# Optimization experiments

Measured on AMD Instinct MI355X. Metric: run time of the kernel, lower is better.

The kernel has to match this reference:

```python
import jax, jax.numpy as jnp
import numpy as np

MUL0, MUL1, SCALARS_OUT = 16, 16, 128
L0, L1 = MUL0, MUL1 * 3            # 16, 48
PATH_NUMEL = MUL0 * MUL1 * SCALARS_OUT  # 32768 per path, two paths
EPS = 1e-5
# e3nn normalization: irrep_normalization='component' -> alpha = dim(ir_out) = 1;
# path_normalization='element' -> divide by sum over paths to same output of mul1*mul2 = 256+256 = 512.
PATH_COEFF = 1.0 / np.sqrt(512.0)
CG_110 = 1.0 / np.sqrt(3.0)  # wigner_3j(1,1,0)[i,j] = delta_ij/sqrt(3) (unit Frobenius norm)


def layer_norm(x, g, b):
    mu = jnp.mean(x, axis=-1, keepdims=True)
    var = jnp.mean(jnp.square(x - mu), axis=-1, keepdims=True)
    return (x - mu) * jax.lax.rsqrt(var + EPS) * g + b


def ff_block(x, g, b, w1, w2, b2):
    # LayerNorm -> Linear(no bias) -> SiLU -> Linear(bias); residual=False in both uses
    h = jax.nn.silu(layer_norm(x, g, b) @ w1)
    return h @ w2 + b2


def setup_inputs() -> dict:
    key = jax.random.key(0)
    ks = jax.random.split(key, 8)
    N = 2048
    return {
        "x": jax.random.normal(ks[0], (N, L0 + L1), dtype=jnp.float32),
        "we_ln_g": jnp.ones((L0,), jnp.float32),
        "we_ln_b": jnp.zeros((L0,), jnp.float32),
        "we_w1": jax.random.normal(ks[1], (L0, 4 * L0), jnp.float32) / np.sqrt(L0),
        "we_w2": jax.random.normal(ks[2], (4 * L0, 2 * PATH_NUMEL), jnp.float32) / np.sqrt(4 * L0),
        "we_b2": jnp.zeros((2 * PATH_NUMEL,), jnp.float32),
        "om_ln_g": jnp.ones((SCALARS_OUT,), jnp.float32),
        "om_ln_b": jnp.zeros((SCALARS_OUT,), jnp.float32),
        "om_w1": jax.random.normal(ks[3], (SCALARS_OUT, 4 * SCALARS_OUT), jnp.float32) / np.sqrt(SCALARS_OUT),
        "om_w2": jax.random.normal(ks[4], (4 * SCALARS_OUT, 1), jnp.float32) / np.sqrt(4 * SCALARS_OUT),
        "om_b2": jnp.zeros((1,), jnp.float32),
    }


def reference(x, we_ln_g, we_ln_b, we_w1, we_w2, we_b2,
              om_ln_g, om_ln_b, om_w1, om_w2, om_b2):
    N = x.shape[0]
    feats = x[:, :L0]                       # [N, 16] scalars (0e)
    x1 = x[:, L0:].reshape(N, MUL1, 3)      # [N, 16, 3] vectors (1o)

    # per-sample tensor-product weights (shared_weights=False)
    w = ff_block(feats, we_ln_g, we_ln_b, we_w1, we_w2, we_b2)  # [N, 65536]
    w0 = w[:, :PATH_NUMEL].reshape(N, MUL0, MUL0, SCALARS_OUT)
    w1 = w[:, PATH_NUMEL:].reshape(N, MUL1, MUL1, SCALARS_OUT)

    # path 0: 0e x 0e -> 0e  (uvw)
    o0 = jnp.einsum('nu,nv,nuvw->nw', feats, feats, w0)
    # path 1: 1o x 1o -> 0e  (uvw, CG = delta_ij/sqrt(3))
    o1 = jnp.einsum('nui,nvi,nuvw->nw', x1, x1, w1) * CG_110
    tp_out = PATH_COEFF * (o0 + o1)          # [N, 128]

    return ff_block(tp_out, om_ln_g, om_ln_b, om_w1, om_w2, om_b2)  # [N, 1]
```

## Files before the change

kernel.cpp:

```cpp
#include <hip/hip_runtime.h>
#include <hip/hip_bf16.h>
#include <cstdint>

#define EPS 1e-5f
#define PATH_COEFF 0.04419417382415922f
#define CG110     0.5773502691896258f

typedef __bf16 v8bf __attribute__((ext_vector_type(8)));
typedef float  v4f  __attribute__((ext_vector_type(4)));
typedef _Float16 v4h __attribute__((ext_vector_type(4)));

static __device__ __forceinline__ unsigned short f2bf(float x){
    unsigned int u = __builtin_bit_cast(unsigned int, x);
    u += 0x7fffu + ((u >> 16) & 1u);
    return (unsigned short)(u >> 16);
}
static __device__ __forceinline__ unsigned short f2h(float x){
    return __builtin_bit_cast(unsigned short, (_Float16)x);
}

__global__ __launch_bounds__(256)
void k_pre(const float* __restrict__ w2, const float* __restrict__ b2,
           unsigned short* __restrict__ Vt2,
           const float* __restrict__ om_w1, unsigned short* __restrict__ w1t,
           const float* __restrict__ x, const float* __restrict__ lng,
           const float* __restrict__ lnb, const float* __restrict__ we_w1,
           unsigned short* __restrict__ Q2, float* __restrict__ Ht, int N)
{
    __shared__ __align__(16) unsigned short tile[32][128];
    int b = blockIdx.x;
    int t = threadIdx.x;

    if (b < 260){
        int k    = b >> 2;
        int slab = b & 3;
        const float* srcbase = (k < 64) ? (w2 + (size_t)k * 65536) : b2;
        for (int chunk = 0; chunk < 4; ++chunk){
            int pbase = slab*128 + chunk*32;
            #pragma unroll
            for (int i = 0; i < 4; ++i){
                int g = t + 256*i;
                int ploc = g >> 5, c4 = g & 31;
                const float4 v = *(const float4*)(srcbase + (size_t)(pbase + ploc)*128 + c4*4);
                unsigned int w0 = (unsigned)f2bf(v.x) | ((unsigned)f2bf(v.y) << 16);
                unsigned int w1 = (unsigned)f2bf(v.z) | ((unsigned)f2bf(v.w) << 16);
                *(uint2*)&tile[ploc][c4*4] = make_uint2(w0, w1);
            }
            __syncthreads();
            int w = t & 127, h = t >> 7;
            int ps = slab*4 + chunk;
            unsigned int words[8];
            #pragma unroll
            for (int g2 = 0; g2 < 8; ++g2)
                words[g2] = (unsigned)tile[h*16 + g2*2][w] | ((unsigned)tile[h*16 + g2*2 + 1][w] << 16);
            unsigned short* dq0 = Vt2 + (((size_t)(k*16 + ps)*4 + 2*h    )*128 + w)*8;
            unsigned short* dq1 = Vt2 + (((size_t)(k*16 + ps)*4 + 2*h + 1)*128 + w)*8;
            *(uint4*)dq0 = make_uint4(words[0], words[1], words[2], words[3]);
            *(uint4*)dq1 = make_uint4(words[4], words[5], words[6], words[7]);
            __syncthreads();
        }
    } else if (b < 264){
        int j0 = (b - 260) * 128;
        for (int chunk = 0; chunk < 4; ++chunk){
            #pragma unroll
            for (int i = 0; i < 4; ++i){
                int g = t + 256*i;
                int wloc = g >> 5, c4 = g & 31;
                int w = chunk*32 + wloc;
                const float4 v = *(const float4*)(om_w1 + (size_t)w*512 + j0 + c4*4);
                unsigned int a = (unsigned)f2bf(v.x) | ((unsigned)f2bf(v.y) << 16);
                unsigned int bb = (unsigned)f2bf(v.z) | ((unsigned)f2bf(v.w) << 16);
                *(uint2*)&tile[wloc][c4*4] = make_uint2(a, bb);
            }
            __syncthreads();
            int jl = t & 127, h = t >> 7;
            unsigned int words[8];
            #pragma unroll
            for (int g2 = 0; g2 < 8; ++g2)
                words[g2] = (unsigned)tile[h*16 + g2*2][jl] | ((unsigned)tile[h*16 + g2*2 + 1][jl] << 16);
            unsigned short* dst = w1t + (size_t)(j0 + jl)*128 + chunk*32 + h*16;
            *(uint4*)dst       = make_uint4(words[0], words[1], words[2], words[3]);
            *(uint4*)(dst + 8) = make_uint4(words[4], words[5], words[6], words[7]);
            __syncthreads();
        }
    } else {
        int wv = t >> 6, lane = t & 63;
        int row = (b - 264)*4 + wv;
        const float* xr = x + (size_t)row * 64;
        float f[16]; float mu = 0.f;
        #pragma unroll
        for (int u = 0; u < 16; ++u){ f[u] = xr[u]; mu += f[u]; }
        mu *= (1.f/16.f);
        float var = 0.f;
        #pragma unroll
        for (int u = 0; u < 16; ++u){ float d = f[u] - mu; var += d*d; }
        var *= (1.f/16.f);
        float inv = rsqrtf(var + EPS);
        float lnf[16];
        #pragma unroll
        for (int u = 0; u < 16; ++u) lnf[u] = (f[u]-mu)*inv*lng[u] + lnb[u];
        float h1 = 0.f;
        #pragma unroll
        for (int u = 0; u < 16; ++u) h1 += lnf[u] * we_w1[u*64 + lane];
        float h = h1 / (1.f + expf(-h1));
        Ht[(size_t)lane * N + row] = h;
        if (lane == 0) Ht[(size_t)64 * N + row] = 1.f;

        union { unsigned short qs[8]; uint4 v; } qu;
        #pragma unroll
        for (int j = 0; j < 8; ++j){
            int p = lane*8 + j;
            float q;
            if (p < 256){
                int u = p >> 4, v = p & 15;
                q = PATH_COEFF * f[u] * f[v];
            } else {
                int pp = p - 256;
                int u = pp >> 4, v = pp & 15;
                const float* ya = xr + 16 + u*3;
                const float* yb = xr + 16 + v*3;
                q = (PATH_COEFF * CG110) * (ya[0]*yb[0] + ya[1]*yb[1] + ya[2]*yb[2]);
            }
            qu.qs[j] = f2bf(q);
        }
        int rb = row >> 6, r64 = row & 63;
        int ps = lane >> 2, quad4 = lane & 3;
        *(uint4*)(Q2 + (((size_t)(rb*16 + ps)*4 + quad4)*64 + r64)*8) = qu.v;
    }
}

__global__ __launch_bounds__(256, 4)
void k_main(const unsigned short* __restrict__ Q2, const unsigned short* __restrict__ Vt2,
            const float* __restrict__ Ht, unsigned short* __restrict__ partial, int N)
{
    __shared__ __align__(16) unsigned short stile[4][64*72];
    int g = blockIdx.x & 7;
    int j = blockIdx.x >> 3;
    int kb, mb;
    if (j < 128){ mb = j >> 3; kb = g*8 + (j & 7); }
    else { if (g != 0) return; mb = j - 128; kb = 64; }

    int tid  = threadIdx.x;
    int lane = tid & 63, wv = tid >> 6;
    int r2 = wv >> 1, c2 = wv & 1;
    int quad = lane >> 4, l16 = lane & 15;
    int rowbase = mb*128 + r2*64;
    int rb = rowbase >> 6;
    int wbase = c2*64;

    const unsigned short* aroot = Q2  + (size_t)rb*32768 + quad*512  + l16*8;
    const unsigned short* broot = Vt2 + (size_t)kb*65536 + quad*1024 + (wbase + l16)*8;

    v4f acc[4][4];
    #pragma unroll
    for (int m=0;m<4;++m)
      #pragma unroll
      for (int n=0;n<4;++n)
        #pragma unroll
        for (int r=0;r<4;++r) acc[m][n][r] = 0.f;

    #pragma unroll 4
    for (int ps = 0; ps < 16; ++ps){
        const unsigned short* ap = aroot + ps*2048;
        const unsigned short* bp = broot + ps*4096;
        v8bf a[4], bb[4];
        #pragma unroll
        for (int m=0;m<4;++m) a[m]  = *(const v8bf*)(ap + m*128);
        #pragma unroll
        for (int n=0;n<4;++n) bb[n] = *(const v8bf*)(bp + n*128);
        #pragma unroll
        for (int m=0;m<4;++m)
          #pragma unroll
          for (int n=0;n<4;++n)
            acc[m][n] = __builtin_amdgcn_mfma_f32_16x16x32_bf16(a[m], bb[n], acc[m][n], 0, 0, 0);
    }

    const float* hp = Ht + (size_t)kb*N + rowbase + quad*4;
    unsigned short* my = stile[wv];
    #pragma unroll
    for (int m=0;m<4;++m){
        v4f hv = *(const v4f*)(hp + m*16);
        #pragma unroll
        for (int n=0;n<4;++n)
          #pragma unroll
          for (int r=0;r<4;++r)
            my[(m*16 + quad*4 + r)*72 + n*16 + l16] = f2h(hv[r]*acc[m][n][r]);
    }
    unsigned short* gp = partial + (size_t)kb*N*128 + (size_t)rowbase*128 + wbase;
    #pragma unroll
    for (int i = 0; i < 8; ++i){
        int row = i*8 + (lane >> 3);
        int c16 = (lane & 7)*8;
        uint4 v = *(const uint4*)&my[row*72 + c16];
        *(uint4*)(gp + (size_t)row*128 + c16) = v;
    }
}

__global__ __launch_bounds__(128)
void k_red(const unsigned short* __restrict__ partial, const float* __restrict__ g,
           const float* __restrict__ b, unsigned short* __restrict__ lnf, int N)
{
    int t = threadIdx.x;
    int row0 = blockIdx.x * 4;
    int rl = t >> 5, w = (t & 31)*4;
    int row = row0 + rl;

    const unsigned short* p0 = partial + (size_t)row*128 + w;
    float s0=0.f, s1=0.f, s2=0.f, s3=0.f;
    #pragma unroll
    for (int sl = 0; sl < 65; ++sl){
        v4h v = *(const v4h*)(p0 + (size_t)sl*N*128);
        s0 += (float)v[0]; s1 += (float)v[1]; s2 += (float)v[2]; s3 += (float)v[3];
    }
    float sum = s0+s1+s2+s3;
    float sq  = s0*s0+s1*s1+s2*s2+s3*s3;
    #pragma unroll
    for (int off=16; off>0; off>>=1){
        sum += __shfl_xor(sum, off, 32);
        sq  += __shfl_xor(sq,  off, 32);
    }
    float mu  = sum * (1.f/128.f);
    float var = sq * (1.f/128.f) - mu*mu;
    float inv = rsqrtf(var + EPS);
    unsigned short o[4];
    o[0] = f2bf((s0-mu)*inv*g[w+0] + b[w+0]);
    o[1] = f2bf((s1-mu)*inv*g[w+1] + b[w+1]);
    o[2] = f2bf((s2-mu)*inv*g[w+2] + b[w+2]);
    o[3] = f2bf((s3-mu)*inv*g[w+3] + b[w+3]);
    *(uint2*)(lnf + (size_t)row*128 + w) = *(uint2*)o;
}

__global__ __launch_bounds__(256)
void k_mlp2(const unsigned short* __restrict__ lnf, const unsigned short* __restrict__ w1t,
            const float* __restrict__ w2, const float* __restrict__ b2,
            float* __restrict__ out, int N)
{
    __shared__ float red2[4][64];
    int tid = threadIdx.x, lane = tid & 63, wv = tid >> 6;
    int quad = lane >> 4, l16 = lane & 15;
    int rowbase = blockIdx.x * 64;
    int jbase = wv * 128;

    v4f acc[4][8];
    #pragma unroll
    for (int m=0;m<4;++m)
      #pragma unroll
      for (int n=0;n<8;++n)
        #pragma unroll
        for (int r=0;r<4;++r) acc[m][n][r] = 0.f;

    #pragma unroll
    for (int ps = 0; ps < 4; ++ps){
        v8bf a[4], bb[8];
        #pragma unroll
        for (int m=0;m<4;++m)
            a[m]  = *(const v8bf*)(lnf + (size_t)(rowbase + m*16 + l16)*128 + ps*32 + quad*8);
        #pragma unroll
        for (int n=0;n<8;++n)
            bb[n] = *(const v8bf*)(w1t + (size_t)(jbase + n*16 + l16)*128 + ps*32 + quad*8);
        #pragma unroll
        for (int m=0;m<4;++m)
          #pragma unroll
          for (int n=0;n<8;++n)
            acc[m][n] = __builtin_amdgcn_mfma_f32_16x16x32_bf16(a[m], bb[n], acc[m][n], 0, 0, 0);
    }

    float w2v[8];
    #pragma unroll
    for (int n=0;n<8;++n) w2v[n] = w2[jbase + n*16 + l16];

    #pragma unroll
    for (int m=0;m<4;++m){
        #pragma unroll
        for (int r=0;r<4;++r){
            float s = 0.f;
            #pragma unroll
            for (int n=0;n<8;++n){
                float v = acc[m][n][r];
                s += (v / (1.f + expf(-v))) * w2v[n];
            }
            #pragma unroll
            for (int off=8; off>0; off>>=1) s += __shfl_xor(s, off, 16);
            if (l16 == 0) red2[wv][m*16 + quad*4 + r] = s;
        }
    }
    __syncthreads();
    if (tid < 64)
        out[rowbase + tid] = red2[0][tid] + red2[1][tid] + red2[2][tid] + red2[3][tid] + b2[0];
}

extern "C" void kernel_launch(void* const* d_in, const int* in_sizes, int n_in,
                              void* d_out, int out_size, void* d_ws, size_t ws_size,
                              hipStream_t stream)
{
    const float* x     = (const float*)d_in[0];
    const float* we_g  = (const float*)d_in[1];
    const float* we_b  = (const float*)d_in[2];
    const float* we_w1 = (const float*)d_in[3];
    const float* we_w2 = (const float*)d_in[4];
    const float* we_b2 = (const float*)d_in[5];
    const float* om_g  = (const float*)d_in[6];
    const float* om_b  = (const float*)d_in[7];
    const float* om_w1 = (const float*)d_in[8];
    const float* om_w2 = (const float*)d_in[9];
    const float* om_b2 = (const float*)d_in[10];

    int N  = in_sizes[0] / 64;

    char* ws = (char*)d_ws;
    size_t offV = 0;
    size_t szV  = (size_t)65*16*4*128*8*2;
    size_t offQ = offV + szV;
    size_t szQ  = (size_t)N*512*2;
    size_t offH = offQ + szQ;
    size_t szH  = (size_t)65*N*4;
    size_t offP = offH + szH;
    size_t szP  = (size_t)65*N*128*2;
    size_t offL = offP + szP;
    size_t szL  = (size_t)N*128*2;
    size_t offW = offL + szL;

    unsigned short* Vt2 = (unsigned short*)(ws + offV);
    unsigned short* Q2  = (unsigned short*)(ws + offQ);
    float* Ht           = (float*)(ws + offH);
    unsigned short* Par = (unsigned short*)(ws + offP);
    unsigned short* Lnf = (unsigned short*)(ws + offL);
    unsigned short* W1t = (unsigned short*)(ws + offW);
    float* out = (float*)d_out;

    hipLaunchKernelGGL(k_pre,  dim3(264 + N/4), dim3(256), 0, stream,
                       we_w2, we_b2, Vt2, om_w1, W1t, x, we_g, we_b, we_w1, Q2, Ht, N);
    hipLaunchKernelGGL(k_main, dim3(144*8),     dim3(256), 0, stream, Q2, Vt2, Ht, Par, N);
    hipLaunchKernelGGL(k_red,  dim3(N/4),       dim3(128), 0, stream, Par, om_g, om_b, Lnf, N);
    hipLaunchKernelGGL(k_mlp2, dim3(N/64),      dim3(256), 0, stream, Lnf, W1t, om_w2, om_b2, out, N);
}
```

Baseline: 145.8 us.

## Stage per-slice weight tile in LDS and process two row tiles per block

k_main now copies the kb weight slice from Vt2 into 64 KB of shared memory in two halves. Each block computes two 128-row tiles against it, so the B operand is reused from LDS instead of being re-read from global/L2 by every row tile. The grid shrinks to 65*8 blocks with launch bounds lowered to 2 per SM. The epilogue stages results through a smaller per-wave LDS buffer with a stride of 66, which can leave 16-byte LDS reads unaligned. Lower occupancy and fewer blocks may reduce latency hiding.

```diff
diff --git a/kernel.cpp b/kernel.cpp
--- a/kernel.cpp
+++ b/kernel.cpp
@@ -129,70 +129,93 @@
     }
 }
 
-__global__ __launch_bounds__(256, 4)
+__global__ __launch_bounds__(256, 2)
 void k_main(const unsigned short* __restrict__ Q2, const unsigned short* __restrict__ Vt2,
             const float* __restrict__ Ht, unsigned short* __restrict__ partial, int N)
 {
-    __shared__ __align__(16) unsigned short stile[4][64*72];
-    int g = blockIdx.x & 7;
-    int j = blockIdx.x >> 3;
-    int kb, mb;
-    if (j < 128){ mb = j >> 3; kb = g*8 + (j & 7); }
-    else { if (g != 0) return; mb = j - 128; kb = 64; }
+    __shared__ __align__(16) unsigned short Bs[32768];
+    int kb = blockIdx.x % 65;
+    int g  = blockIdx.x / 65;
 
     int tid  = threadIdx.x;
     int lane = tid & 63, wv = tid >> 6;
     int r2 = wv >> 1, c2 = wv & 1;
     int quad = lane >> 4, l16 = lane & 15;
-    int rowbase = mb*128 + r2*64;
-    int rb = rowbase >> 6;
     int wbase = c2*64;
 
-    const unsigned short* aroot = Q2  + (size_t)rb*32768 + quad*512  + l16*8;
-    const unsigned short* broot = Vt2 + (size_t)kb*65536 + quad*1024 + (wbase + l16)*8;
-
-    v4f acc[4][4];
-    #pragma unroll
-    for (int m=0;m<4;++m)
+    v4f acc[2][4][4];
+    #pragma unroll
+    for (int mi=0;mi<2;++mi)
       #pragma unroll
-      for (int n=0;n<4;++n)
-        #pragma unroll
-        for (int r=0;r<4;++r) acc[m][n][r] = 0.f;
-
-    #pragma unroll 4
-    for (int ps = 0; ps < 16; ++ps){
-        const unsigned short* ap = aroot + ps*2048;
-        const unsigned short* bp = broot + ps*4096;
-        v8bf a[4], bb[4];
-        #pragma unroll
-        for (int m=0;m<4;++m) a[m]  = *(const v8bf*)(ap + m*128);
-        #pragma unroll
-        for (int n=0;n<4;++n) bb[n] = *(const v8bf*)(bp + n*128);
-        #pragma unroll
-        for (int m=0;m<4;++m)
-          #pragma unroll
-          for (int n=0;n<4;++n)
-            acc[m][n] = __builtin_amdgcn_mfma_f32_16x16x32_bf16(a[m], bb[n], acc[m][n], 0, 0, 0);
-    }
-
-    const float* hp = Ht + (size_t)kb*N + rowbase + quad*4;
-    unsigned short* my = stile[wv];
-    #pragma unroll
-    for (int m=0;m<4;++m){
-        v4f hv = *(const v4f*)(hp + m*16);
+      for (int m=0;m<4;++m)
         #pragma unroll
         for (int n=0;n<4;++n)
           #pragma unroll
-          for (int r=0;r<4;++r)
-            my[(m*16 + quad*4 + r)*72 + n*16 + l16] = f2h(hv[r]*acc[m][n][r]);
-    }
-    unsigned short* gp = partial + (size_t)kb*N*128 + (size_t)rowbase*128 + wbase;
-    #pragma unroll
-    for (int i = 0; i < 8; ++i){
-        int row = i*8 + (lane >> 3);
-        int c16 = (lane & 7)*8;
-        uint4 v = *(const uint4*)&my[row*72 + c16];
-        *(uint4*)(gp + (size_t)row*128 + c16) = v;
+          for (int r=0;r<4;++r) acc[mi][m][n][r] = 0.f;
+
+    const unsigned short* bsrc = Vt2 + (size_t)kb*65536;
+
+    for (int half = 0; half < 2; ++half){
+        __syncthreads();
+        const uint4* s4 = (const uint4*)(bsrc + half*32768);
+        uint4* d4 = (uint4*)Bs;
+        #pragma unroll
+        for (int i = 0; i < 16; ++i)
+            d4[tid + i*256] = s4[tid + i*256];
+        __syncthreads();
+
+        #pragma unroll
+        for (int mi = 0; mi < 2; ++mi){
+            int rowbase = (g*2 + mi)*128 + r2*64;
+            int rb = rowbase >> 6;
+            const unsigned short* aroot = Q2 + (size_t)rb*32768 + half*16384 + quad*512 + l16*8;
+            #pragma unroll
+            for (int pc = 0; pc < 2; ++pc){
+                v8bf a[4][4];
+                #pragma unroll
+                for (int ps = 0; ps < 4; ++ps)
+                    #pragma unroll
+                    for (int m = 0; m < 4; ++m)
+                        a[ps][m] = *(const v8bf*)(aroot + (pc*4 + ps)*2048 + m*128);
+                #pragma unroll
+                for (int ps = 0; ps < 4; ++ps){
+                    int ps8 = pc*4 + ps;
+                    const unsigned short* bp = Bs + ((ps8*4 + quad)*128 + wbase + l16)*8;
+                    v8bf bb[4];
+                    #pragma unroll
+                    for (int n = 0; n < 4; ++n) bb[n] = *(const v8bf*)(bp + n*128);
+                    #pragma unroll
+                    for (int m = 0; m < 4; ++m)
+                      #pragma unroll
+                      for (int n = 0; n < 4; ++n)
+                        acc[mi][m][n] = __builtin_amdgcn_mfma_f32_16x16x32_bf16(a[ps][m], bb[n], acc[mi][m][n], 0, 0, 0);
+                }
+            }
+        }
+    }
+
+    __syncthreads();
+    unsigned short* Es = Bs + wv*1056;
+    #pragma unroll
+    for (int mi = 0; mi < 2; ++mi){
+        int rowbase = (g*2 + mi)*128 + r2*64;
+        const float* hp = Ht + (size_t)kb*N + rowbase + quad*4;
+        #pragma unroll
+        for (int m = 0; m < 4; ++m){
+            v4f hv = *(const v4f*)(hp + m*16);
+            #pragma unroll
+            for (int n = 0; n < 4; ++n)
+              #pragma unroll
+              for (int r = 0; r < 4; ++r)
+                Es[(quad*4 + r)*66 + n*16 + l16] = f2h(hv[r]*acc[mi][m][n][r]);
+            unsigned short* gp = partial + (size_t)kb*N*128 + (size_t)(rowbase + m*16)*128 + wbase;
+            #pragma unroll
+            for (int jj = 0; jj < 2; ++jj){
+                int idx = lane*2 + jj;
+                int rr = idx >> 3, cc = idx & 7;
+                *(uint4*)(gp + (size_t)rr*128 + cc*8) = *(const uint4*)(Es + rr*66 + cc*8);
+            }
+        }
     }
 }
 
@@ -330,7 +353,7 @@
 
     hipLaunchKernelGGL(k_pre,  dim3(264 + N/4), dim3(256), 0, stream,
                        we_w2, we_b2, Vt2, om_w1, W1t, x, we_g, we_b, we_w1, Q2, Ht, N);
-    hipLaunchKernelGGL(k_main, dim3(144*8),     dim3(256), 0, stream, Q2, Vt2, Ht, Par, N);
+    hipLaunchKernelGGL(k_main, dim3(65*8),      dim3(256), 0, stream, Q2, Vt2, Ht, Par, N);
     hipLaunchKernelGGL(k_red,  dim3(N/4),       dim3(128), 0, stream, Par, om_g, om_b, Lnf, N);
     hipLaunchKernelGGL(k_mlp2, dim3(N/64),      dim3(256), 0, stream, Lnf, W1t, om_w2, om_b2, out, N);
 }
```

Result: slower. 170.0 us (+16.6%).

## Shrink k_main blocks to 64x128 tiles, stage output per 16 rows, use nontemporal stores

Applied to the files above, without the earlier changes.

Blocks of k_main now use two waves covering 64 rows by 128 columns instead of four waves covering 128x128. The grid becomes a plain 65x32 mapping, replacing the grouped kb/mb scheme that left idle blocks. The LDS staging tile shrinks to 16 rows per wave and is written out in chunks with nontemporal stores, and k_red reads the partials with nontemporal loads. The goal is lower LDS use and more resident blocks, plus less cache pollution from the large partial buffer. The cost is that each block reuses its A tile across fewer waves, and the stores are issued in smaller chunks.

```diff
diff --git a/kernel.cpp b/kernel.cpp
--- a/kernel.cpp
+++ b/kernel.cpp
@@ -9,6 +9,8 @@
 typedef __bf16 v8bf __attribute__((ext_vector_type(8)));
 typedef float  v4f  __attribute__((ext_vector_type(4)));
 typedef _Float16 v4h __attribute__((ext_vector_type(4)));
+typedef unsigned int v4u __attribute__((ext_vector_type(4)));
+typedef unsigned int v2u __attribute__((ext_vector_type(2)));
 
 static __device__ __forceinline__ unsigned short f2bf(float x){
     unsigned int u = __builtin_bit_cast(unsigned int, x);
@@ -129,26 +131,21 @@
     }
 }
 
-__global__ __launch_bounds__(256, 4)
+__global__ __launch_bounds__(128, 4)
 void k_main(const unsigned short* __restrict__ Q2, const unsigned short* __restrict__ Vt2,
             const float* __restrict__ Ht, unsigned short* __restrict__ partial, int N)
 {
-    __shared__ __align__(16) unsigned short stile[4][64*72];
-    int g = blockIdx.x & 7;
-    int j = blockIdx.x >> 3;
-    int kb, mb;
-    if (j < 128){ mb = j >> 3; kb = g*8 + (j & 7); }
-    else { if (g != 0) return; mb = j - 128; kb = 64; }
+    __shared__ __align__(16) unsigned short Es[2][16*66];
+    int kb = blockIdx.x % 65;
+    int mb = blockIdx.x / 65;
 
     int tid  = threadIdx.x;
     int lane = tid & 63, wv = tid >> 6;
-    int r2 = wv >> 1, c2 = wv & 1;
     int quad = lane >> 4, l16 = lane & 15;
-    int rowbase = mb*128 + r2*64;
-    int rb = rowbase >> 6;
-    int wbase = c2*64;
-
-    const unsigned short* aroot = Q2  + (size_t)rb*32768 + quad*512  + l16*8;
+    int rowbase = mb * 64;
+    int wbase = wv * 64;
+
+    const unsigned short* aroot = Q2  + (size_t)mb*32768 + quad*512  + l16*8;
     const unsigned short* broot = Vt2 + (size_t)kb*65536 + quad*1024 + (wbase + l16)*8;
 
     v4f acc[4][4];
@@ -176,23 +173,23 @@
     }
 
     const float* hp = Ht + (size_t)kb*N + rowbase + quad*4;
-    unsigned short* my = stile[wv];
-    #pragma unroll
-    for (int m=0;m<4;++m){
+    unsigned short* my = Es[wv];
+    unsigned short* gp = partial + (size_t)kb*N*128 + (size_t)rowbase*128 + wbase;
+    #pragma unroll
+    for (int m = 0; m < 4; ++m){
         v4f hv = *(const v4f*)(hp + m*16);
         #pragma unroll
-        for (int n=0;n<4;++n)
+        for (int n = 0; n < 4; ++n)
           #pragma unroll
-          for (int r=0;r<4;++r)
-            my[(m*16 + quad*4 + r)*72 + n*16 + l16] = f2h(hv[r]*acc[m][n][r]);
-    }
-    unsigned short* gp = partial + (size_t)kb*N*128 + (size_t)rowbase*128 + wbase;
-    #pragma unroll
-    for (int i = 0; i < 8; ++i){
-        int row = i*8 + (lane >> 3);
-        int c16 = (lane & 7)*8;
-        uint4 v = *(const uint4*)&my[row*72 + c16];
-        *(uint4*)(gp + (size_t)row*128 + c16) = v;
+          for (int r = 0; r < 4; ++r)
+            my[(quad*4 + r)*66 + n*16 + l16] = f2h(hv[r]*acc[m][n][r]);
+        #pragma unroll
+        for (int jj = 0; jj < 2; ++jj){
+            int idx = lane*2 + jj;
+            int rr = idx >> 3, cc = idx & 7;
+            v4u v = *(const v4u*)(Es[wv] + rr*66 + cc*8);
+            __builtin_nontemporal_store(v, (v4u*)(gp + (size_t)(m*16 + rr)*128 + cc*8));
+        }
     }
 }
 
@@ -209,8 +206,9 @@
     float s0=0.f, s1=0.f, s2=0.f, s3=0.f;
     #pragma unroll
     for (int sl = 0; sl < 65; ++sl){
-        v4h v = *(const v4h*)(p0 + (size_t)sl*N*128);
-        s0 += (float)v[0]; s1 += (float)v[1]; s2 += (float)v[2]; s3 += (float)v[3];
+        union { v2u u; v4h h; } cv;
+        cv.u = __builtin_nontemporal_load((const v2u*)(p0 + (size_t)sl*N*128));
+        s0 += (float)cv.h[0]; s1 += (float)cv.h[1]; s2 += (float)cv.h[2]; s3 += (float)cv.h[3];
     }
     float sum = s0+s1+s2+s3;
     float sq  = s0*s0+s1*s1+s2*s2+s3*s3;
@@ -330,7 +328,7 @@
 
     hipLaunchKernelGGL(k_pre,  dim3(264 + N/4), dim3(256), 0, stream,
                        we_w2, we_b2, Vt2, om_w1, W1t, x, we_g, we_b, we_w1, Q2, Ht, N);
-    hipLaunchKernelGGL(k_main, dim3(144*8),     dim3(256), 0, stream, Q2, Vt2, Ht, Par, N);
+    hipLaunchKernelGGL(k_main, dim3(32*65),     dim3(128), 0, stream, Q2, Vt2, Ht, Par, N);
     hipLaunchKernelGGL(k_red,  dim3(N/4),       dim3(128), 0, stream, Par, om_g, om_b, Lnf, N);
     hipLaunchKernelGGL(k_mlp2, dim3(N/64),      dim3(256), 0, stream, Lnf, W1t, om_w2, om_b2, out, N);
 }
```

After: 151.9 us. +4.2%, slower.
